# Performance work log

Hardware: AMD Instinct MI355X
Metric: run time of the kernel (lower is better)

## Reference

```python
import jax, jax.numpy as jnp
import numpy as np

B, N, C = 8, 2048, 64  # batch, num nodes, channels
DENSITY = 0.01


def setup_inputs() -> dict:
    key = jax.random.key(0)
    k = jax.random.split(key, 8)
    x = jax.random.normal(k[0], (B, N, C), dtype=jnp.float32)

    # --- replicate sym_norm_Adj(Adj_matrix) + row softmax from __init__ ---
    W = (jax.random.uniform(k[1], (N, N)) < DENSITY).astype(jnp.float32)
    W = W + 0.5 * jnp.eye(N, dtype=jnp.float32)          # W + 0.5*I
    deg = jnp.sum((W != 0.0).astype(jnp.float32), axis=1)  # row nonzero counts
    A = jnp.sqrt(deg)[:, None] * W * jnp.sqrt(deg)[None, :]  # sqrt(D) W sqrt(D)
    A = jax.nn.softmax(A, axis=1)

    s = 1.0 / np.sqrt(C)
    Wq = jax.random.normal(k[2], (C, C), dtype=jnp.float32) * s   # stored as (in,out)
    Wk = jax.random.normal(k[3], (C, C), dtype=jnp.float32) * s
    Wv = jax.random.normal(k[4], (C, N), dtype=jnp.float32) * s   # c_in -> num_node
    theta_w = jax.random.normal(k[5], (C, C), dtype=jnp.float32) * s
    theta_b = jnp.zeros((C,), dtype=jnp.float32)
    alpha = jnp.array([0.95], dtype=jnp.float32)
    beta = jnp.array([0.95], dtype=jnp.float32)
    return {"x": x, "A": A, "Wq": Wq, "Wk": Wk, "Wv": Wv,
            "theta_w": theta_w, "theta_b": theta_b, "alpha": alpha, "beta": beta}


def reference(x, A, Wq, Wk, Wv, theta_w, theta_b, alpha, beta):
    # Spatial_Attention_layer
    Q = x @ Wq                                   # (B,N,C)
    K = x @ Wk                                   # (B,N,C)
    V = x @ Wv                                   # (B,N,N)
    score = jnp.einsum('bnc,bmc->bnm', Q, K)     # (B,N,N)
    score = jax.nn.softmax(score, axis=1)        # softmax over dim=1 (as in torch code)
    spat = jnp.einsum('bnm,bmk->bnk', score, V)  # (B,N,N) spatial attention

    # einsum('nn,bnc->bnc', A, x) == diag(A) broadcast-multiply
    static_out = jnp.diagonal(A)[None, :, None] * x  # (B,N,C)

    # dy_adj = A @ spat; einsum('bnn,bnc->bnc', dy_adj, x) uses only diag(dy_adj)
    dy_diag = jnp.einsum('nj,bjn->bn', A, spat)      # (B,N), avoids (B,N,N) intermediate
    dy_out = (dy_diag[:, :, None] * x) @ theta_w + theta_b  # Theta1 linear

    out = jax.nn.relu(alpha[0] * static_out + beta[0] * dy_out)
    return out
```

## Files before the change

kernel.cpp:

```cpp
#include <hip/hip_runtime.h>

constexpr int Bb = 8;
constexpr int Nn = 2048;
constexpr int Cc = 64;
constexpr int CAPS = 192;

typedef __attribute__((ext_vector_type(4))) float f32x4;
typedef __attribute__((ext_vector_type(16))) float f32x16;
typedef __attribute__((ext_vector_type(8))) short bf16x8;
typedef __attribute__((ext_vector_type(4))) unsigned u32x4;

__device__ inline unsigned short f2bf(float f){
  unsigned u = __builtin_bit_cast(unsigned, f);
  unsigned r = (u + 0x7FFFu + ((u>>16)&1u)) >> 16;
  return (unsigned short)r;
}
__device__ inline float bf2f(unsigned short h){
  unsigned u = ((unsigned)h)<<16; return __builtin_bit_cast(float,u);
}
__device__ inline unsigned pk2(float a, float b){
  return (unsigned)f2bf(a) | ((unsigned)f2bf(b)<<16);
}

typedef __attribute__((address_space(1))) unsigned GU32;
typedef __attribute__((address_space(3))) unsigned LU32;
__device__ inline void load_lds16(const void* g, void* l){
  __builtin_amdgcn_global_load_lds((const GU32*)g, (LU32*)l, 16, 0, 0);
}

__device__ inline size_t qk_chunk(int b, int s, int q, int l){
  return ((((size_t)b*64 + s)*4 + q)*64 + l)*8;
}
__device__ inline size_t xz_chunk(int b, int mq, int cb, int l){
  return ((((size_t)b*128 + mq)*2 + cb)*64 + l)*8;
}

#define MFMA32(a,b,c) __builtin_amdgcn_mfma_f32_32x32x16_bf16(a,b,c,0,0,0)

__global__ __launch_bounds__(256) void mega_k(
    const float* __restrict__ x, const float* __restrict__ A,
    const float* __restrict__ Wq, const float* __restrict__ Wk,
    const float* __restrict__ Tw, const float* __restrict__ Wv,
    unsigned short* __restrict__ Qhi, unsigned short* __restrict__ Qlo,
    unsigned short* __restrict__ Khi, unsigned short* __restrict__ Klo,
    float* __restrict__ xt, float* __restrict__ Xp,
    float* __restrict__ r_, float* __restrict__ diagA, int* __restrict__ cnt,
    int* __restrict__ idx, float* __restrict__ val,
    float* __restrict__ WvT){
  __shared__ __attribute__((aligned(16))) char smem[65792];
  int blk = blockIdx.x; int t = threadIdx.x;

  if(blk < 256){
    float* wql = (float*)smem;
    float* wkl = wql + 4096;
    float* twl = wkl + 4096;
    float (*xr)[64] = (float(*)[64])(twl + 4096);
    float* xsl = (float*)(xr + 64);
    #pragma unroll
    for(int i=0;i<4;i++){
      *(f32x4*)&wql[i*1024+t*4] = *(const f32x4*)&Wq[i*1024+t*4];
      *(f32x4*)&wkl[i*1024+t*4] = *(const f32x4*)&Wk[i*1024+t*4];
      *(f32x4*)&twl[i*1024+t*4] = *(const f32x4*)&Tw[i*1024+t*4];
    }
    if(t<64) xsl[t]=0.f;
    long long row0 = (long long)blk*64;
    int r = t>>4, q = t&15, c0 = q*4;
    #pragma unroll
    for(int i=0;i<4;i++){
      int row = i*16 + r;
      *(f32x4*)&xr[row][c0] = *(const f32x4*)&x[(row0+row)*Cc + c0];
    }
    __syncthreads();
    f32x4 aq[4], ak[4], at4[4];
    #pragma unroll
    for(int g=0;g<4;g++){ aq[g]=(f32x4){0,0,0,0}; ak[g]=(f32x4){0,0,0,0}; at4[g]=(f32x4){0,0,0,0}; }
    for(int kk=0;kk<64;kk++){
      f32x4 wq4 = *(const f32x4*)&wql[kk*64+c0];
      f32x4 wk4 = *(const f32x4*)&wkl[kk*64+c0];
      f32x4 wt4 = *(const f32x4*)&twl[kk*64+c0];
      #pragma unroll
      for(int g=0;g<4;g++){
        float xv = xr[g*16+r][kk];
        aq[g] += xv*wq4; ak[g] += xv*wk4; at4[g] += xv*wt4;
      }
    }
    float xsp[4] = {0.f,0.f,0.f,0.f};
    int q2 = c0>>4, hb = (c0>>3)&1, cs = c0&7;
    #pragma unroll
    for(int g=0;g<4;g++){
      #pragma unroll
      for(int d=0;d<4;d++) xsp[d] += xr[g*16+r][c0+d];
      long long rg = row0 + g*16 + r;
      unsigned long long hq=0,lq=0,hk=0,lk=0;
      #pragma unroll
      for(int d=0;d<4;d++){
        float v = aq[g][d];
        unsigned short h = f2bf(v); unsigned short lo2 = f2bf(v - bf2f(h));
        hq |= (unsigned long long)h << (16*d); lq |= (unsigned long long)lo2 << (16*d);
        v = ak[g][d];
        h = f2bf(v); lo2 = f2bf(v - bf2f(h));
        hk |= (unsigned long long)h << (16*d); lk |= (unsigned long long)lo2 << (16*d);
      }
      int b2 = (int)(rg>>11); int s2 = ((int)rg>>5)&63;
      int l2 = ((int)rg&31) + 32*hb;
      size_t off = qk_chunk(b2, s2, q2, l2) + cs;
      *(unsigned long long*)&Qhi[off] = hq;
      *(unsigned long long*)&Qlo[off] = lq;
      *(unsigned long long*)&Khi[off] = hk;
      *(unsigned long long*)&Klo[off] = lk;
      *(f32x4*)&xt[rg*Cc + c0] = at4[g];
    }
    __syncthreads();
    #pragma unroll
    for(int d=0;d<4;d++) atomicAdd(&xsl[c0+d], xsp[d]);
    __syncthreads();
    if(t<64) Xp[blk*64+t] = xsl[t];
  } else if(blk < 768){
    int n = (blk-256)*4 + (t>>6); int l = t&63;
    const float* row = A + (size_t)n*Nn;
    float mn = 1e30f;
    for(int j=l;j<Nn;j+=64) mn = fminf(mn, row[j]);
    #pragma unroll
    for(int off=32;off>=1;off>>=1) mn = fminf(mn, __shfl_xor(mn,off));
    float thr = mn*1.3f;
    int bse=0;
    for(int j0=0;j0<Nn;j0+=64){
      float v = row[j0+l];
      bool f = v>thr;
      unsigned long long m = __ballot(f);
      int pos = __popcll(m & ((1ull<<l)-1ull));
      if(f && bse+pos<CAPS){ idx[n*CAPS+bse+pos]=j0+l; val[n*CAPS+bse+pos]=v-mn; }
      bse += __popcll(m);
    }
    if(l==0){ r_[n]=mn; diagA[n]=row[n]; cnt[n] = bse<CAPS? bse : CAPS; }
  } else {
    float (*tile)[65] = (float(*)[65])smem;
    int n0 = (blk-768)*64;
    for(int i=0;i<16;i++){
      int cc = i*4 + (t>>6); int nn2 = t&63;
      tile[cc][nn2] = Wv[(size_t)cc*Nn + n0 + nn2];
    }
    __syncthreads();
    for(int i=0;i<16;i++){
      int nn2 = i*4 + (t>>6); int cc = t&63;
      WvT[(size_t)(n0+nn2)*Cc + cc] = tile[cc][nn2];
    }
  }
}

__global__ __launch_bounds__(256,2) void zpass_k(
    const unsigned short* __restrict__ Qhi, const unsigned short* __restrict__ Qlo,
    const unsigned short* __restrict__ Khi, const unsigned short* __restrict__ Klo,
    float* __restrict__ Zp){
  __shared__ uint4 stg[2][512];
  int id = blockIdx.x;
  int b = id&7; int mg = (id>>3)&15; int jq = id>>7;
  int t = threadIdx.x, w = t>>6, l = t&63;
  int mt = mg*4 + w;
  bf16x8 Kh[4], Kl4[4];
  #pragma unroll
  for(int q=0;q<4;q++){
    Kh[q]  = *(const bf16x8*)(Khi + qk_chunk(b, mt, q, l));
    Kl4[q] = *(const bf16x8*)(Klo + qk_chunk(b, mt, q, l));
  }
  char* wbase0 = (char*)&stg[0][0] + (t>>6)*1024;
  char* wbase1 = (char*)&stg[1][0] + (t>>6)*1024;
  {
    int s = jq*16;
    load_lds16(Qhi + qk_chunk(b,s,0,0) + t*8, wbase0);
    load_lds16(Qlo + qk_chunk(b,s,0,0) + t*8, wbase0 + 4096);
  }
  __syncthreads();
  float zacc = 0.f;
  for(int it=0; it<16; it++){
    int buf = it&1;
    if(it+1<16){
      int s = jq*16 + it + 1;
      char* wb = buf? wbase0 : wbase1;
      load_lds16(Qhi + qk_chunk(b,s,0,0) + t*8, wb);
      load_lds16(Qlo + qk_chunk(b,s,0,0) + t*8, wb + 4096);
    }
    f32x16 sa, sb;
    #pragma unroll
    for(int r=0;r<16;r++){ sa[r]=0.f; sb[r]=0.f; }
    #pragma unroll
    for(int q=0;q<4;q++){
      bf16x8 Qh4 = *(const bf16x8*)&stg[buf][q*64 + l];
      bf16x8 Ql4 = *(const bf16x8*)&stg[buf][256 + q*64 + l];
      sa = MFMA32(Qh4, Kh[q],  sa);
      sb = MFMA32(Ql4, Kh[q],  sb);
      sb = MFMA32(Qh4, Kl4[q], sb);
    }
    float p = 0.f;
    #pragma unroll
    for(int r=0;r<16;r++) p += __expf(sa[r]+sb[r]);
    zacc += p;
    __syncthreads();
  }
  zacc += __shfl_down(zacc, 32);
  if(l<32) Zp[((size_t)(jq*8 + b))*Nn + mt*32 + l] = zacc;
}

__global__ __launch_bounds__(256) void xzt_k(const float* __restrict__ x,
    const float* __restrict__ Zp, unsigned short* __restrict__ xzf){
  __shared__ float tile[64][65];
  __shared__ float izl[64];
  int id = blockIdx.x; int b = id&7; int mt = id>>3;
  int m0 = mt*64; int t = threadIdx.x;
  for(int i=0;i<16;i++){
    int mm = i*4 + (t>>6); int cc = t&63;
    tile[mm][cc] = x[((size_t)b*Nn + m0+mm)*Cc + cc];
  }
  if(t<64){
    float z = 0.f;
    #pragma unroll
    for(int jq=0;jq<4;jq++) z += Zp[((size_t)(jq*8 + b))*Nn + m0 + t];
    izl[t] = 1.0f/z;
  }
  __syncthreads();
  #pragma unroll
  for(int i=0;i<2;i++){
    int k2 = i*256 + t; int mg = k2>>6; int c = k2&63;
    int mloc = mg*8;
    unsigned u0 = pk2(tile[mloc+0][c]*izl[mloc+0], tile[mloc+1][c]*izl[mloc+1]);
    unsigned u1 = pk2(tile[mloc+2][c]*izl[mloc+2], tile[mloc+3][c]*izl[mloc+3]);
    unsigned u2 = pk2(tile[mloc+4][c]*izl[mloc+4], tile[mloc+5][c]*izl[mloc+5]);
    unsigned u3 = pk2(tile[mloc+6][c]*izl[mloc+6], tile[mloc+7][c]*izl[mloc+7]);
    u32x4 uu = {u0,u1,u2,u3};
    int mq = (m0 + mloc)>>4; int cb = c>>5; int l2 = (c&31) + 32*(mg&1);
    *(u32x4*)(xzf + xz_chunk(b, mq, cb, l2)) = uu;
  }
}

__global__ __launch_bounds__(256,2) void fused_k(
    const unsigned short* __restrict__ Qhi, const unsigned short* __restrict__ Qlo,
    const unsigned short* __restrict__ Khi, const unsigned short* __restrict__ Klo,
    const unsigned short* __restrict__ xzf, float* __restrict__ Pp){
  __shared__ uint4 stg[2][768];
  int id = blockIdx.x;
  int b = id&7; int jb = (id>>3)&15; int mq4 = id>>7;
  int t = threadIdx.x, w = t>>6, l = t&63, lr = l&31, hh = l>>5;
  int js = jb*4 + w;
  bf16x8 Qh4[4], Ql4[4];
  #pragma unroll
  for(int q=0;q<4;q++){
    Qh4[q] = *(const bf16x8*)(Qhi + qk_chunk(b, js, q, l));
    Ql4[q] = *(const bf16x8*)(Qlo + qk_chunk(b, js, q, l));
  }
  char* wbase0 = (char*)&stg[0][0] + (t>>6)*1024;
  char* wbase1 = (char*)&stg[1][0] + (t>>6)*1024;
  {
    int s = mq4*16;
    load_lds16(Khi + qk_chunk(b,s,0,0) + t*8, wbase0);
    load_lds16(Klo + qk_chunk(b,s,0,0) + t*8, wbase0 + 4096);
    load_lds16(xzf + xz_chunk(b,2*s,0,0) + t*8, wbase0 + 8192);
  }
  __syncthreads();
  f32x16 pa0, pa1;
  #pragma unroll
  for(int r=0;r<16;r++){ pa0[r]=0.f; pa1[r]=0.f; }
  for(int it=0; it<16; it++){
    int buf = it&1;
    if(it+1<16){
      int s = mq4*16 + it + 1;
      char* wb = buf? wbase0 : wbase1;
      load_lds16(Khi + qk_chunk(b,s,0,0) + t*8, wb);
      load_lds16(Klo + qk_chunk(b,s,0,0) + t*8, wb + 4096);
      load_lds16(xzf + xz_chunk(b,2*s,0,0) + t*8, wb + 8192);
    }
    f32x16 sa, sb;
    #pragma unroll
    for(int r=0;r<16;r++){ sa[r]=0.f; sb[r]=0.f; }
    #pragma unroll
    for(int q=0;q<4;q++){
      bf16x8 Kh4 = *(const bf16x8*)&stg[buf][q*64 + l];
      bf16x8 Kl4 = *(const bf16x8*)&stg[buf][256 + q*64 + l];
      sa = MFMA32(Kh4, Qh4[q], sa);
      sb = MFMA32(Kl4, Qh4[q], sb);
      sb = MFMA32(Kh4, Ql4[q], sb);
    }
    bf16x8 b00 = *(const bf16x8*)&stg[buf][512 + l];
    bf16x8 b10 = *(const bf16x8*)&stg[buf][512 + 64 + l];
    bf16x8 b01 = *(const bf16x8*)&stg[buf][512 + 128 + l];
    bf16x8 b11 = *(const bf16x8*)&stg[buf][512 + 192 + l];
    unsigned wd0,wd1,wd2,wd3,wd4,wd5,wd6,wd7;
    {
      unsigned x0 = pk2(__expf(sa[0]+sb[0]),   __expf(sa[1]+sb[1]));
      unsigned x1 = pk2(__expf(sa[2]+sb[2]),   __expf(sa[3]+sb[3]));
      unsigned y0 = pk2(__expf(sa[4]+sb[4]),   __expf(sa[5]+sb[5]));
      unsigned y1 = pk2(__expf(sa[6]+sb[6]),   __expf(sa[7]+sb[7]));
      asm("v_permlane32_swap_b32 %0, %1" : "+v"(x0), "+v"(y0));
      asm("v_permlane32_swap_b32 %0, %1" : "+v"(x1), "+v"(y1));
      wd0=x0; wd1=x1; wd2=y0; wd3=y1;
      unsigned x2 = pk2(__expf(sa[8]+sb[8]),   __expf(sa[9]+sb[9]));
      unsigned x3 = pk2(__expf(sa[10]+sb[10]), __expf(sa[11]+sb[11]));
      unsigned y2 = pk2(__expf(sa[12]+sb[12]), __expf(sa[13]+sb[13]));
      unsigned y3 = pk2(__expf(sa[14]+sb[14]), __expf(sa[15]+sb[15]));
      asm("v_permlane32_swap_b32 %0, %1" : "+v"(x2), "+v"(y2));
      asm("v_permlane32_swap_b32 %0, %1" : "+v"(x3), "+v"(y3));
      wd4=x2; wd5=x3; wd6=y2; wd7=y3;
    }
    u32x4 u1 = {wd0,wd1,wd2,wd3};
    u32x4 u2 = {wd4,wd5,wd6,wd7};
    bf16x8 f1 = __builtin_bit_cast(bf16x8, u1);
    bf16x8 f2 = __builtin_bit_cast(bf16x8, u2);
    pa0 = MFMA32(f1, b00, pa0);
    pa0 = MFMA32(f2, b01, pa0);
    pa1 = MFMA32(f1, b10, pa1);
    pa1 = MFMA32(f2, b11, pa1);
    __syncthreads();
  }
  float* Pb = Pp + ((size_t)(mq4*8 + b)*Nn + js*32)*Cc;
  #pragma unroll
  for(int r=0;r<16;r++){
    int jr = (r&3) + 8*(r>>2) + 4*hh;
    Pb[(size_t)jr*Cc + lr]      = pa0[r];
    Pb[(size_t)jr*Cc + 32 + lr] = pa1[r];
  }
}

__global__ __launch_bounds__(256) void psum_k(const float* __restrict__ Pp,
                                              float* __restrict__ P){
  size_t i = ((size_t)blockIdx.x*256 + threadIdx.x)*4;
  const size_t st = (size_t)Bb*Nn*Cc;
  f32x4 a = *(const f32x4*)(Pp + i);
  f32x4 b = *(const f32x4*)(Pp + st + i);
  f32x4 c = *(const f32x4*)(Pp + 2*st + i);
  f32x4 d = *(const f32x4*)(Pp + 3*st + i);
  *(f32x4*)(P + i) = (a+b)+(c+d);
}

__global__ __launch_bounds__(256) void final_k(const float* __restrict__ x,
    const float* __restrict__ xt, const float* __restrict__ P,
    const float* __restrict__ WvT, const float* __restrict__ Xp,
    const float* __restrict__ r_, const float* __restrict__ diagA,
    const int* __restrict__ cnt, const int* __restrict__ idx,
    const float* __restrict__ val, const float* __restrict__ tb,
    const float* __restrict__ alp, const float* __restrict__ bet,
    float* __restrict__ out){
  int t=threadIdx.x; int l=t&63;
  int bn = blockIdx.x*4 + (t>>6);
  int b = bn>>11, n = bn&2047;
  float wv = WvT[n*Cc+l];
  float xs = 0.f;
  const float* xpb = Xp + (size_t)b*32*Cc;
  #pragma unroll 8
  for(int p=0;p<32;p++) xs += xpb[p*Cc + l];
  float tacc = r_[n]*xs;
  int cn = cnt[n];
  const float* Pb = P + (size_t)b*Nn*Cc;
  const int* ix = idx + n*CAPS;
  const float* vl = val + n*CAPS;
  for(int k=0;k<cn;k++)
    tacc += vl[k] * Pb[(size_t)ix[k]*Cc + l];
  float d = wv*tacc;
  #pragma unroll
  for(int off=32;off>=1;off>>=1) d += __shfl_xor(d,off);
  size_t g = (size_t)bn*Cc + l;
  float o = alp[0]*diagA[n]*x[g] + bet[0]*(d*xt[g] + tb[l]);
  out[g] = fmaxf(o,0.f);
}

extern "C" void kernel_launch(void* const* d_in, const int* in_sizes, int n_in,
                              void* d_out, int out_size, void* d_ws, size_t ws_size,
                              hipStream_t stream){
  const float* x  = (const float*)d_in[0];
  const float* A  = (const float*)d_in[1];
  const float* Wq = (const float*)d_in[2];
  const float* Wk = (const float*)d_in[3];
  const float* Wv = (const float*)d_in[4];
  const float* Tw = (const float*)d_in[5];
  const float* tb = (const float*)d_in[6];
  const float* alp= (const float*)d_in[7];
  const float* bet= (const float*)d_in[8];
  float* out = (float*)d_out;

  char* base = (char*)d_ws; size_t off=0;
  auto al=[&](size_t sz)->void*{ void* q = base+off; off=(off+sz+255)&~(size_t)255; return q; };
  unsigned short* Qhi=(unsigned short*)al((size_t)Bb*Nn*Cc*2);
  unsigned short* Qlo=(unsigned short*)al((size_t)Bb*Nn*Cc*2);
  unsigned short* Khi=(unsigned short*)al((size_t)Bb*Nn*Cc*2);
  unsigned short* Klo=(unsigned short*)al((size_t)Bb*Nn*Cc*2);
  float* xt  =(float*)al((size_t)Bb*Nn*Cc*4);
  float* Pp  =(float*)al((size_t)4*Bb*Nn*Cc*4);
  float* P   =(float*)al((size_t)Bb*Nn*Cc*4);
  float* Zp  =(float*)al((size_t)4*Bb*Nn*4);
  float* Xp  =(float*)al((size_t)256*Cc*4);
  float* WvT =(float*)al((size_t)Nn*Cc*4);
  float* r_  =(float*)al((size_t)Nn*4);
  float* dgA =(float*)al((size_t)Nn*4);
  int*   cnt =(int*)al((size_t)Nn*4);
  int*   idx =(int*)al((size_t)Nn*CAPS*4);
  float* val =(float*)al((size_t)Nn*CAPS*4);
  unsigned short* xzf=(unsigned short*)al((size_t)Bb*Cc*Nn*2);
  (void)ws_size;

  mega_k<<<800, 256, 0, stream>>>(x, A, Wq, Wk, Tw, Wv,
      Qhi, Qlo, Khi, Klo, xt, Xp, r_, dgA, cnt, idx, val, WvT);
  zpass_k<<<512, 256, 0, stream>>>(Qhi,Qlo,Khi,Klo,Zp);
  xzt_k<<<256, 256, 0, stream>>>(x,Zp,xzf);
  fused_k<<<512, 256, 0, stream>>>(Qhi,Qlo,Khi,Klo,xzf,Pp);
  psum_k<<<(int)((size_t)Bb*Nn*Cc/4/256), 256, 0, stream>>>(Pp,P);
  final_k<<<Bb*Nn/4, 256, 0, stream>>>(x,xt,P,WvT,Xp,r_,dgA,cnt,idx,val,tb,alp,bet,out);
}
```

Before: 107.4 us.

## Fold softmax normalization into exp and split m-range eightfold for more blocks

Removes the xzt_k kernel. mega_k now writes an unnormalized bf16 x layout, and fused_k applies the softmax denominator as -log(Z) added inside the exponent, reading Zp itself. zpass_k and fused_k also split the reduction dimension into 8 parts instead of 4, doubling the grid to 1024 blocks. This costs twice the partial-sum buffer traffic in psum_k and a redundant Z reduction plus log per fused block. The exponent now uses the normalized score directly, which slightly changes the bf16 rounding of the probabilities.

```diff
diff --git a/kernel.cpp b/kernel.cpp
--- a/kernel.cpp
+++ b/kernel.cpp
@@ -46,7 +46,7 @@
     float* __restrict__ xt, float* __restrict__ Xp,
     float* __restrict__ r_, float* __restrict__ diagA, int* __restrict__ cnt,
     int* __restrict__ idx, float* __restrict__ val,
-    float* __restrict__ WvT){
+    float* __restrict__ WvT, unsigned short* __restrict__ xf){
   __shared__ __attribute__((aligned(16))) char smem[65792];
   int blk = blockIdx.x; int t = threadIdx.x;
 
@@ -115,6 +115,21 @@
     for(int d=0;d<4;d++) atomicAdd(&xsl[c0+d], xsp[d]);
     __syncthreads();
     if(t<64) Xp[blk*64+t] = xsl[t];
+    {
+      int b2 = blk>>5; int m0 = (blk&31)*64;
+      #pragma unroll
+      for(int i=0;i<2;i++){
+        int k2 = i*256 + t; int mg2 = k2>>6; int c = k2&63;
+        int mloc = mg2*8;
+        unsigned u0 = pk2(xr[mloc+0][c], xr[mloc+1][c]);
+        unsigned u1 = pk2(xr[mloc+2][c], xr[mloc+3][c]);
+        unsigned u2 = pk2(xr[mloc+4][c], xr[mloc+5][c]);
+        unsigned u3 = pk2(xr[mloc+6][c], xr[mloc+7][c]);
+        u32x4 uu = {u0,u1,u2,u3};
+        int mq = (m0 + mloc)>>4; int cb = c>>5; int l2 = (c&31) + 32*(mg2&1);
+        *(u32x4*)(xf + xz_chunk(b2, mq, cb, l2)) = uu;
+      }
+    }
   } else if(blk < 768){
     int n = (blk-256)*4 + (t>>6); int l = t&63;
     const float* row = A + (size_t)n*Nn;
@@ -166,16 +181,16 @@
   char* wbase0 = (char*)&stg[0][0] + (t>>6)*1024;
   char* wbase1 = (char*)&stg[1][0] + (t>>6)*1024;
   {
-    int s = jq*16;
+    int s = jq*8;
     load_lds16(Qhi + qk_chunk(b,s,0,0) + t*8, wbase0);
     load_lds16(Qlo + qk_chunk(b,s,0,0) + t*8, wbase0 + 4096);
   }
   __syncthreads();
   float zacc = 0.f;
-  for(int it=0; it<16; it++){
+  for(int it=0; it<8; it++){
     int buf = it&1;
-    if(it+1<16){
-      int s = jq*16 + it + 1;
+    if(it+1<8){
+      int s = jq*8 + it + 1;
       char* wb = buf? wbase0 : wbase1;
       load_lds16(Qhi + qk_chunk(b,s,0,0) + t*8, wb);
       load_lds16(Qlo + qk_chunk(b,s,0,0) + t*8, wb + 4096);
@@ -201,46 +216,24 @@
   if(l<32) Zp[((size_t)(jq*8 + b))*Nn + mt*32 + l] = zacc;
 }
 
-__global__ __launch_bounds__(256) void xzt_k(const float* __restrict__ x,
-    const float* __restrict__ Zp, unsigned short* __restrict__ xzf){
-  __shared__ float tile[64][65];
-  __shared__ float izl[64];
-  int id = blockIdx.x; int b = id&7; int mt = id>>3;
-  int m0 = mt*64; int t = threadIdx.x;
-  for(int i=0;i<16;i++){
-    int mm = i*4 + (t>>6); int cc = t&63;
-    tile[mm][cc] = x[((size_t)b*Nn + m0+mm)*Cc + cc];
-  }
-  if(t<64){
-    float z = 0.f;
-    #pragma unroll
-    for(int jq=0;jq<4;jq++) z += Zp[((size_t)(jq*8 + b))*Nn + m0 + t];
-    izl[t] = 1.0f/z;
-  }
-  __syncthreads();
-  #pragma unroll
-  for(int i=0;i<2;i++){
-    int k2 = i*256 + t; int mg = k2>>6; int c = k2&63;
-    int mloc = mg*8;
-    unsigned u0 = pk2(tile[mloc+0][c]*izl[mloc+0], tile[mloc+1][c]*izl[mloc+1]);
-    unsigned u1 = pk2(tile[mloc+2][c]*izl[mloc+2], tile[mloc+3][c]*izl[mloc+3]);
-    unsigned u2 = pk2(tile[mloc+4][c]*izl[mloc+4], tile[mloc+5][c]*izl[mloc+5]);
-    unsigned u3 = pk2(tile[mloc+6][c]*izl[mloc+6], tile[mloc+7][c]*izl[mloc+7]);
-    u32x4 uu = {u0,u1,u2,u3};
-    int mq = (m0 + mloc)>>4; int cb = c>>5; int l2 = (c&31) + 32*(mg&1);
-    *(u32x4*)(xzf + xz_chunk(b, mq, cb, l2)) = uu;
-  }
-}
-
 __global__ __launch_bounds__(256,2) void fused_k(
     const unsigned short* __restrict__ Qhi, const unsigned short* __restrict__ Qlo,
     const unsigned short* __restrict__ Khi, const unsigned short* __restrict__ Klo,
-    const unsigned short* __restrict__ xzf, float* __restrict__ Pp){
+    const unsigned short* __restrict__ xf, const float* __restrict__ Zp,
+    float* __restrict__ Pp){
   __shared__ uint4 stg[2][768];
+  __shared__ float lniz[256];
   int id = blockIdx.x;
-  int b = id&7; int jb = (id>>3)&15; int mq4 = id>>7;
+  int b = id&7; int jb = (id>>3)&15; int mo = id>>7;
   int t = threadIdx.x, w = t>>6, l = t&63, lr = l&31, hh = l>>5;
   int js = jb*4 + w;
+  {
+    int m = mo*256 + t;
+    float z = 0.f;
+    #pragma unroll
+    for(int p=0;p<8;p++) z += Zp[((size_t)(p*8 + b))*Nn + m];
+    lniz[t] = -__logf(z);
+  }
   bf16x8 Qh4[4], Ql4[4];
   #pragma unroll
   for(int q=0;q<4;q++){
@@ -250,23 +243,23 @@
   char* wbase0 = (char*)&stg[0][0] + (t>>6)*1024;
   char* wbase1 = (char*)&stg[1][0] + (t>>6)*1024;
   {
-    int s = mq4*16;
+    int s = mo*8;
     load_lds16(Khi + qk_chunk(b,s,0,0) + t*8, wbase0);
     load_lds16(Klo + qk_chunk(b,s,0,0) + t*8, wbase0 + 4096);
-    load_lds16(xzf + xz_chunk(b,2*s,0,0) + t*8, wbase0 + 8192);
+    load_lds16(xf + xz_chunk(b,2*s,0,0) + t*8, wbase0 + 8192);
   }
   __syncthreads();
   f32x16 pa0, pa1;
   #pragma unroll
   for(int r=0;r<16;r++){ pa0[r]=0.f; pa1[r]=0.f; }
-  for(int it=0; it<16; it++){
+  for(int it=0; it<8; it++){
     int buf = it&1;
-    if(it+1<16){
-      int s = mq4*16 + it + 1;
+    if(it+1<8){
+      int s = mo*8 + it + 1;
       char* wb = buf? wbase0 : wbase1;
       load_lds16(Khi + qk_chunk(b,s,0,0) + t*8, wb);
       load_lds16(Klo + qk_chunk(b,s,0,0) + t*8, wb + 4096);
-      load_lds16(xzf + xz_chunk(b,2*s,0,0) + t*8, wb + 8192);
+      load_lds16(xf + xz_chunk(b,2*s,0,0) + t*8, wb + 8192);
     }
     f32x16 sa, sb;
     #pragma unroll
@@ -283,19 +276,25 @@
     bf16x8 b10 = *(const bf16x8*)&stg[buf][512 + 64 + l];
     bf16x8 b01 = *(const bf16x8*)&stg[buf][512 + 128 + l];
     bf16x8 b11 = *(const bf16x8*)&stg[buf][512 + 192 + l];
+    float e[16];
+    #pragma unroll
+    for(int r=0;r<16;r++){
+      int mrow = (r&3) + 8*(r>>2) + 4*hh;
+      e[r] = __expf(sa[r] + sb[r] + lniz[it*32 + mrow]);
+    }
     unsigned wd0,wd1,wd2,wd3,wd4,wd5,wd6,wd7;
     {
-      unsigned x0 = pk2(__expf(sa[0]+sb[0]),   __expf(sa[1]+sb[1]));
-      unsigned x1 = pk2(__expf(sa[2]+sb[2]),   __expf(sa[3]+sb[3]));
-      unsigned y0 = pk2(__expf(sa[4]+sb[4]),   __expf(sa[5]+sb[5]));
-      unsigned y1 = pk2(__expf(sa[6]+sb[6]),   __expf(sa[7]+sb[7]));
+      unsigned x0 = pk2(e[0],  e[1]);
+      unsigned x1 = pk2(e[2],  e[3]);
+      unsigned y0 = pk2(e[4],  e[5]);
+      unsigned y1 = pk2(e[6],  e[7]);
       asm("v_permlane32_swap_b32 %0, %1" : "+v"(x0), "+v"(y0));
       asm("v_permlane32_swap_b32 %0, %1" : "+v"(x1), "+v"(y1));
       wd0=x0; wd1=x1; wd2=y0; wd3=y1;
-      unsigned x2 = pk2(__expf(sa[8]+sb[8]),   __expf(sa[9]+sb[9]));
-      unsigned x3 = pk2(__expf(sa[10]+sb[10]), __expf(sa[11]+sb[11]));
-      unsigned y2 = pk2(__expf(sa[12]+sb[12]), __expf(sa[13]+sb[13]));
-      unsigned y3 = pk2(__expf(sa[14]+sb[14]), __expf(sa[15]+sb[15]));
+      unsigned x2 = pk2(e[8],  e[9]);
+      unsigned x3 = pk2(e[10], e[11]);
+      unsigned y2 = pk2(e[12], e[13]);
+      unsigned y3 = pk2(e[14], e[15]);
       asm("v_permlane32_swap_b32 %0, %1" : "+v"(x2), "+v"(y2));
       asm("v_permlane32_swap_b32 %0, %1" : "+v"(x3), "+v"(y3));
       wd4=x2; wd5=x3; wd6=y2; wd7=y3;
@@ -310,7 +309,7 @@
     pa1 = MFMA32(f2, b11, pa1);
     __syncthreads();
   }
-  float* Pb = Pp + ((size_t)(mq4*8 + b)*Nn + js*32)*Cc;
+  float* Pb = Pp + ((size_t)(mo*8 + b)*Nn + js*32)*Cc;
   #pragma unroll
   for(int r=0;r<16;r++){
     int jr = (r&3) + 8*(r>>2) + 4*hh;
@@ -323,11 +322,11 @@
                                               float* __restrict__ P){
   size_t i = ((size_t)blockIdx.x*256 + threadIdx.x)*4;
   const size_t st = (size_t)Bb*Nn*Cc;
-  f32x4 a = *(const f32x4*)(Pp + i);
-  f32x4 b = *(const f32x4*)(Pp + st + i);
-  f32x4 c = *(const f32x4*)(Pp + 2*st + i);
-  f32x4 d = *(const f32x4*)(Pp + 3*st + i);
-  *(f32x4*)(P + i) = (a+b)+(c+d);
+  f32x4 s0 = *(const f32x4*)(Pp + i)        + *(const f32x4*)(Pp + st + i);
+  f32x4 s1 = *(const f32x4*)(Pp + 2*st + i) + *(const f32x4*)(Pp + 3*st + i);
+  f32x4 s2 = *(const f32x4*)(Pp + 4*st + i) + *(const f32x4*)(Pp + 5*st + i);
+  f32x4 s3 = *(const f32x4*)(Pp + 6*st + i) + *(const f32x4*)(Pp + 7*st + i);
+  *(f32x4*)(P + i) = (s0+s1)+(s2+s3);
 }
 
 __global__ __launch_bounds__(256) void final_k(const float* __restrict__ x,
@@ -382,9 +381,9 @@
   unsigned short* Khi=(unsigned short*)al((size_t)Bb*Nn*Cc*2);
   unsigned short* Klo=(unsigned short*)al((size_t)Bb*Nn*Cc*2);
   float* xt  =(float*)al((size_t)Bb*Nn*Cc*4);
-  float* Pp  =(float*)al((size_t)4*Bb*Nn*Cc*4);
+  float* Pp  =(float*)al((size_t)8*Bb*Nn*Cc*4);
   float* P   =(float*)al((size_t)Bb*Nn*Cc*4);
-  float* Zp  =(float*)al((size_t)4*Bb*Nn*4);
+  float* Zp  =(float*)al((size_t)8*Bb*Nn*4);
   float* Xp  =(float*)al((size_t)256*Cc*4);
   float* WvT =(float*)al((size_t)Nn*Cc*4);
   float* r_  =(float*)al((size_t)Nn*4);
@@ -392,14 +391,13 @@
   int*   cnt =(int*)al((size_t)Nn*4);
   int*   idx =(int*)al((size_t)Nn*CAPS*4);
   float* val =(float*)al((size_t)Nn*CAPS*4);
-  unsigned short* xzf=(unsigned short*)al((size_t)Bb*Cc*Nn*2);
+  unsigned short* xf=(unsigned short*)al((size_t)Bb*Cc*Nn*2);
   (void)ws_size;
 
   mega_k<<<800, 256, 0, stream>>>(x, A, Wq, Wk, Tw, Wv,
-      Qhi, Qlo, Khi, Klo, xt, Xp, r_, dgA, cnt, idx, val, WvT);
-  zpass_k<<<512, 256, 0, stream>>>(Qhi,Qlo,Khi,Klo,Zp);
-  xzt_k<<<256, 256, 0, stream>>>(x,Zp,xzf);
-  fused_k<<<512, 256, 0, stream>>>(Qhi,Qlo,Khi,Klo,xzf,Pp);
+      Qhi, Qlo, Khi, Klo, xt, Xp, r_, dgA, cnt, idx, val, WvT, xf);
+  zpass_k<<<1024, 256, 0, stream>>>(Qhi,Qlo,Khi,Klo,Zp);
+  fused_k<<<1024, 256, 0, stream>>>(Qhi,Qlo,Khi,Klo,xf,Zp,Pp);
   psum_k<<<(int)((size_t)Bb*Nn*Cc/4/256), 256, 0, stream>>>(Pp,P);
   final_k<<<Bb*Nn/4, 256, 0, stream>>>(x,xt,P,WvT,Xp,r_,dgA,cnt,idx,val,tb,alp,bet,out);
 }
```

Measured after the change: 109.8 us. 2.3% more time.
